# Kernel tuning notes

Measured on AMD Instinct MI355X. Metric: run time of the kernel, lower is better.

The kernel has to match this reference:

```python
import jax, jax.numpy as jnp
import numpy as np

N_NODES = 100000


def _gin_layer(x, edge_index, Wa, ba, Wb, bb):
    # GINConv, eps=0: h_i = MLP(x_i + sum_{j->i} x_j)
    src, dst = edge_index[0], edge_index[1]
    agg = jax.ops.segment_sum(x[src], dst, num_segments=N_NODES)  # [N, d]
    h = x + agg
    h = jax.nn.relu(h @ Wa + ba) @ Wb + bb
    return h


def setup_inputs() -> dict:
    key = jax.random.key(0)
    ks = jax.random.split(key, 8)
    d_in, d_h, E = 128, 128, 1600000
    scale_in = 1.0 / np.sqrt(d_in)
    scale_h = 1.0 / np.sqrt(d_h)
    return {
        "x": jax.random.normal(ks[0], (N_NODES, d_in), dtype=jnp.float32),
        "edge_index": jax.random.randint(ks[1], (2, E), 0, N_NODES, dtype=jnp.int64),
        "batch": jnp.zeros((N_NODES,), dtype=jnp.int64),
        "W1a": jax.random.normal(ks[2], (d_in, d_h), dtype=jnp.float32) * scale_in,
        "b1a": jnp.zeros((d_h,), dtype=jnp.float32),
        "W1b": jax.random.normal(ks[3], (d_h, d_h), dtype=jnp.float32) * scale_h,
        "b1b": jnp.zeros((d_h,), dtype=jnp.float32),
        "W2a": jax.random.normal(ks[4], (d_h, d_h), dtype=jnp.float32) * scale_h,
        "b2a": jnp.zeros((d_h,), dtype=jnp.float32),
        "W2b": jax.random.normal(ks[5], (d_h, d_h), dtype=jnp.float32) * scale_h,
        "b2b": jnp.zeros((d_h,), dtype=jnp.float32),
    }


def reference(x, edge_index, batch, W1a, b1a, W1b, b1b, W2a, b2a, W2b, b2b):
    h = jax.nn.relu(_gin_layer(x, edge_index, W1a, b1a, W1b, b1b))
    h = jax.nn.relu(_gin_layer(h, edge_index, W2a, b2a, W2b, b2b))
    return h
```

## Files before the change

### kernel.cpp

```cpp
#include <hip/hip_runtime.h>
#include <hip/hip_bf16.h>

#define D 128
#define EPB 4096
#define CAP 6144

typedef float f32x4 __attribute__((ext_vector_type(4)));
typedef float f32x2 __attribute__((ext_vector_type(2)));
typedef short short8 __attribute__((ext_vector_type(8)));


__device__ __forceinline__ unsigned bf16_rtn_bits(float x) {
    unsigned u = __float_as_uint(x);
    return (u + 0x7fffu + ((u >> 16) & 1u)) >> 16;
}

__device__ __forceinline__ f32x2 pkadd(f32x2 a, f32x2 b) {
    f32x2 d;
    asm("v_pk_add_f32 %0, %1, %2" : "=v"(d) : "v"(a), "v"(b));
    return d;
}

__device__ __forceinline__ void addbf8p(f32x2* acc, uint4 v) {
    f32x2 p0 = {__uint_as_float(v.x << 16), __uint_as_float(v.x & 0xffff0000u)};
    f32x2 p1 = {__uint_as_float(v.y << 16), __uint_as_float(v.y & 0xffff0000u)};
    f32x2 p2 = {__uint_as_float(v.z << 16), __uint_as_float(v.z & 0xffff0000u)};
    f32x2 p3 = {__uint_as_float(v.w << 16), __uint_as_float(v.w & 0xffff0000u)};
    acc[0] = pkadd(acc[0], p0);
    acc[1] = pkadd(acc[1], p1);
    acc[2] = pkadd(acc[2], p2);
    acc[3] = pkadd(acc[3], p3);
}


__global__ __launch_bounds__(256) void k_xtobf(const float4* __restrict__ X, uint4* __restrict__ O,
                                               int n8, int* __restrict__ gz, int nzero) {
    int i = blockIdx.x * 256 + threadIdx.x;
    if (i < nzero) gz[i] = 0;
    if (i >= n8) return;
    float4 a = X[2 * i], b = X[2 * i + 1];
    uint4 o;
    o.x = bf16_rtn_bits(a.x) | (bf16_rtn_bits(a.y) << 16);
    o.y = bf16_rtn_bits(a.z) | (bf16_rtn_bits(a.w) << 16);
    o.z = bf16_rtn_bits(b.x) | (bf16_rtn_bits(b.y) << 16);
    o.w = bf16_rtn_bits(b.z) | (bf16_rtn_bits(b.w) << 16);
    O[i] = o;
}

__global__ void k_wsplit4(const float* __restrict__ W1a, const float* __restrict__ W1b,
                          const float* __restrict__ W2a, const float* __restrict__ W2b,
                          unsigned short* __restrict__ Wt) {
    int m = blockIdx.x >> 6;
    int i = (blockIdx.x & 63) * 256 + threadIdx.x;
    const float* W = (m == 0) ? W1a : (m == 1) ? W1b : (m == 2) ? W2a : W2b;
    int k = i >> 7, n = i & 127;
    Wt[m * 16384 + n * 128 + k] = (unsigned short)bf16_rtn_bits(W[i]);
}


__global__ __launch_bounds__(256) void k_bin(const int* __restrict__ src,
                                             const int* __restrict__ dst, int E,
                                             int* __restrict__ gCursor,
                                             unsigned* __restrict__ binned) {
    __shared__ int cnt[512];
    __shared__ int offs[512];
    __shared__ int c2[512];
    __shared__ int gOff[512];
    __shared__ int s[256];
    __shared__ unsigned staged[EPB];
    __shared__ unsigned short bo[EPB];
    int t = threadIdx.x;
    cnt[t] = 0; cnt[t + 256] = 0;
    c2[t] = 0; c2[t + 256] = 0;
    __syncthreads();

    unsigned pk[EPB / 256];
    int bk[EPB / 256];
    int e0 = blockIdx.x * EPB;
#pragma unroll
    for (int i = 0; i < EPB / 256; ++i) {
        int e = e0 + i * 256 + t;
        int b = -1; unsigned p = 0;
        if (e < E) {
            int dv = dst[e], sv = src[e];
            b = dv >> 8;
            p = ((unsigned)sv << 8) | (unsigned)(dv & 255);
            atomicAdd(&cnt[b], 1);
        }
        pk[i] = p; bk[i] = b;
    }
    __syncthreads();
    int v0 = cnt[2 * t], v1 = cnt[2 * t + 1];
    int ps = v0 + v1;
    s[t] = ps;
    __syncthreads();
    for (int off = 1; off < 256; off <<= 1) {
        int tv = (t >= off) ? s[t - off] : 0;
        __syncthreads();
        s[t] += tv;
        __syncthreads();
    }
    int ex = s[t] - ps;
    offs[2 * t] = ex;
    offs[2 * t + 1] = ex + v0;
    if (cnt[2 * t])     gOff[2 * t]     = atomicAdd(&gCursor[2 * t], cnt[2 * t]);
    if (cnt[2 * t + 1]) gOff[2 * t + 1] = atomicAdd(&gCursor[2 * t + 1], cnt[2 * t + 1]);
    __syncthreads();
#pragma unroll
    for (int i = 0; i < EPB / 256; ++i) {
        int b = bk[i];
        if (b >= 0) {
            int p = offs[b] + atomicAdd(&c2[b], 1);
            staged[p] = pk[i];
            bo[p] = (unsigned short)b;
        }
    }
    __syncthreads();
    int total = s[255];
    for (int p = t; p < total; p += 256) {
        int b = bo[p];
        binned[(size_t)b * CAP + gOff[b] + (p - offs[b])] = staged[p];
    }
}

__global__ __launch_bounds__(256) void k_csr(const unsigned* __restrict__ binned,
                                             const int* __restrict__ bucketCnt,
                                             int* __restrict__ alloc,
                                             int2* __restrict__ rowse,
                                             int* __restrict__ colA,
                                             int Nn) {
    __shared__ int hist[256], loc[256], cur[256], s[256];
    __shared__ int baseSh;
    int t = threadIdx.x, b = blockIdx.x;
    int n = bucketCnt[b];
    const unsigned* bp = binned + (size_t)b * CAP;
    hist[t] = 0; cur[t] = 0;
    __syncthreads();
    for (int i = t; i < n; i += 256) atomicAdd(&hist[bp[i] & 255u], 1);
    __syncthreads();
    int v = hist[t];
    s[t] = v;
    __syncthreads();
    for (int off = 1; off < 256; off <<= 1) {
        int tv = (t >= off) ? s[t - off] : 0;
        __syncthreads();
        s[t] += tv;
        __syncthreads();
    }
    loc[t] = s[t] - v;
    if (t == 255) baseSh = atomicAdd(alloc, s[255]);
    __syncthreads();
    int base = baseSh;
    int node = b * 256 + t;
    if (node < Nn) rowse[node] = make_int2(base + loc[t], base + loc[t] + v);
    for (int i = t; i < n; i += 256) {
        unsigned w = bp[i];
        int dl = (int)(w & 255u);
        int p = atomicAdd(&cur[dl], 1);
        colA[base + loc[dl] + p] = (int)(w >> 8);
    }
}


__global__ __launch_bounds__(256) void agg_bf16(const unsigned short* __restrict__ X,
                                                const int2* __restrict__ rowse,
                                                const int* __restrict__ colA,
                                                unsigned short* __restrict__ H, int nnodes) {
    int node = blockIdx.x * 4 + (threadIdx.x >> 6);
    if (node >= nnodes) return;
    int lane = threadIdx.x & 63;
    int qt = lane >> 4, slot = lane & 15;
    const uint4* x4 = (const uint4*)X;
    size_t base = (size_t)node * 16 + slot;

    int2 se = rowse[node];
    int e = se.x, end = se.y;

    f32x2 acc[4] = {{0.f, 0.f}, {0.f, 0.f}, {0.f, 0.f}, {0.f, 0.f}};
    f32x2 acc2[4] = {{0.f, 0.f}, {0.f, 0.f}, {0.f, 0.f}, {0.f, 0.f}};
    if (qt == 0) addbf8p(acc, x4[base]);

    for (; e + 16 <= end; e += 16) {
        int s0 = colA[e + qt];
        int s1 = colA[e + 4 + qt];
        int s2 = colA[e + 8 + qt];
        int s3 = colA[e + 12 + qt];
        uint4 v0 = x4[(size_t)s0 * 16 + slot];
        uint4 v1 = x4[(size_t)s1 * 16 + slot];
        uint4 v2 = x4[(size_t)s2 * 16 + slot];
        uint4 v3 = x4[(size_t)s3 * 16 + slot];
        addbf8p(acc, v0);
        addbf8p(acc2, v1);
        addbf8p(acc, v2);
        addbf8p(acc2, v3);
    }
    if (e + 8 <= end) {
        int s0 = colA[e + qt];
        int s1 = colA[e + 4 + qt];
        uint4 v0 = x4[(size_t)s0 * 16 + slot];
        uint4 v1 = x4[(size_t)s1 * 16 + slot];
        addbf8p(acc, v0);
        addbf8p(acc2, v1);
        e += 8;
    }
    for (; e < end; e += 4) {
        int idx = e + qt;
        if (idx < end) {
            int s = colA[idx];
            addbf8p(acc, x4[(size_t)s * 16 + slot]);
        }
    }
    float a8[8];
#pragma unroll
    for (int j = 0; j < 4; ++j) {
        f32x2 t = pkadd(acc[j], acc2[j]);
        a8[2 * j] = t[0];
        a8[2 * j + 1] = t[1];
    }
#pragma unroll
    for (int j = 0; j < 8; ++j) {
        a8[j] += __shfl_xor(a8[j], 16);
        a8[j] += __shfl_xor(a8[j], 32);
    }
    if (qt == 0) {
        uint4 o;
        o.x = bf16_rtn_bits(a8[0]) | (bf16_rtn_bits(a8[1]) << 16);
        o.y = bf16_rtn_bits(a8[2]) | (bf16_rtn_bits(a8[3]) << 16);
        o.z = bf16_rtn_bits(a8[4]) | (bf16_rtn_bits(a8[5]) << 16);
        o.w = bf16_rtn_bits(a8[6]) | (bf16_rtn_bits(a8[7]) << 16);
        ((uint4*)H)[base] = o;
    }
}


template <bool OUT_BF16>
__global__ __launch_bounds__(256) void mlp_mfma(const unsigned short* __restrict__ Hb,
                                                const unsigned short* __restrict__ WaT,
                                                const float* __restrict__ ba,
                                                const unsigned short* __restrict__ WbT,
                                                const float* __restrict__ bb,
                                                void* __restrict__ OutP, int nrows) {
    __shared__ unsigned short sh[64 * 128];
    const int tid = threadIdx.x;
    const int wv = tid >> 6, l = tid & 63, q = l >> 4, cl = l & 15;
    const int ntiles = (nrows + 63) >> 6;

    short8 B1[2][4], B2[2][4];
    float bva[2], bvb[2];
#pragma unroll
    for (int cf = 0; cf < 2; ++cf) {
        const unsigned short* wa = WaT + (size_t)(wv * 32 + cf * 16 + cl) * 128 + q * 8;
        const unsigned short* wb = WbT + (size_t)(wv * 32 + cf * 16 + cl) * 128 + q * 8;
#pragma unroll
        for (int kk = 0; kk < 4; ++kk) {
            B1[cf][kk] = *(const short8*)(wa + kk * 32);
            B2[cf][kk] = *(const short8*)(wb + kk * 32);
        }
        bva[cf] = ba[wv * 32 + cf * 16 + cl];
        bvb[cf] = bb[wv * 32 + cf * 16 + cl];
    }

    for (int tile = blockIdx.x; tile < ntiles; tile += gridDim.x) {
        const int rows0 = tile * 64;
        const int nvalid = min(64, nrows - rows0);

        {
            const uint4* src = (const uint4*)(Hb + (size_t)rows0 * 128);
#pragma unroll
            for (int it = 0; it < 4; ++it) {
                int idx = it * 256 + tid;
                int row = idx >> 4, s16 = idx & 15;
                uint4 v = {0u, 0u, 0u, 0u};
                if (row < nvalid) v = src[idx];
                int byteoff = (row << 8) + ((s16 << 4) ^ ((row & 7) << 4));
                *(uint4*)((char*)sh + byteoff) = v;
            }
        }
        __syncthreads();

        f32x4 acc[4][2];
#pragma unroll
        for (int cf = 0; cf < 2; ++cf) {
            f32x4 a = {bva[cf], bva[cf], bva[cf], bva[cf]};
#pragma unroll
            for (int m = 0; m < 4; ++m) acc[m][cf] = a;
        }
#pragma unroll
        for (int kk = 0; kk < 4; ++kk) {
            short8 a[4];
#pragma unroll
            for (int m = 0; m < 4; ++m) {
                int row = m * 16 + cl;
                int byteoff = (row << 8) + ((kk * 64 + q * 16) ^ ((row & 7) << 4));
                a[m] = *(const short8*)((const char*)sh + byteoff);
            }
#pragma unroll
            for (int m = 0; m < 4; ++m)
#pragma unroll
                for (int cf = 0; cf < 2; ++cf)
                    acc[m][cf] = __builtin_amdgcn_mfma_f32_16x16x32_bf16(a[m], B1[cf][kk], acc[m][cf], 0, 0, 0);
        }
        __syncthreads();

#pragma unroll
        for (int m = 0; m < 4; ++m)
#pragma unroll
            for (int cf = 0; cf < 2; ++cf)
#pragma unroll
                for (int r = 0; r < 4; ++r) {
                    int row = m * 16 + q * 4 + r;
                    int col = wv * 32 + cf * 16 + cl;
                    int byteoff = (row << 8) + ((col * 2) ^ ((row & 7) << 4));
                    *(unsigned short*)((char*)sh + byteoff) =
                        (unsigned short)bf16_rtn_bits(fmaxf(acc[m][cf][r], 0.f));
                }
        __syncthreads();

#pragma unroll
        for (int cf = 0; cf < 2; ++cf) {
            f32x4 a = {bvb[cf], bvb[cf], bvb[cf], bvb[cf]};
#pragma unroll
            for (int m = 0; m < 4; ++m) acc[m][cf] = a;
        }
#pragma unroll
        for (int kk = 0; kk < 4; ++kk) {
            short8 a[4];
#pragma unroll
            for (int m = 0; m < 4; ++m) {
                int row = m * 16 + cl;
                int byteoff = (row << 8) + ((kk * 64 + q * 16) ^ ((row & 7) << 4));
                a[m] = *(const short8*)((const char*)sh + byteoff);
            }
#pragma unroll
            for (int m = 0; m < 4; ++m)
#pragma unroll
                for (int cf = 0; cf < 2; ++cf)
                    acc[m][cf] = __builtin_amdgcn_mfma_f32_16x16x32_bf16(a[m], B2[cf][kk], acc[m][cf], 0, 0, 0);
        }

#pragma unroll
        for (int m = 0; m < 4; ++m)
#pragma unroll
            for (int cf = 0; cf < 2; ++cf)
#pragma unroll
                for (int r = 0; r < 4; ++r) {
                    int row = m * 16 + q * 4 + r;
                    if (row < nvalid) {
                        float v = fmaxf(acc[m][cf][r], 0.f);
                        size_t gi = ((size_t)rows0 + row) * 128 + wv * 32 + cf * 16 + cl;
                        if (OUT_BF16)
                            ((unsigned short*)OutP)[gi] = (unsigned short)bf16_rtn_bits(v);
                        else
                            ((float*)OutP)[gi] = v;
                    }
                }
        __syncthreads();
    }
}


extern "C" void kernel_launch(void* const* d_in, const int* in_sizes, int n_in,
                              void* d_out, int out_size, void* d_ws, size_t ws_size,
                              hipStream_t stream) {
    const float* x  = (const float*)d_in[0];
    const int*   ei = (const int*)d_in[1];
    const float* W1a = (const float*)d_in[3];
    const float* b1a = (const float*)d_in[4];
    const float* W1b = (const float*)d_in[5];
    const float* b1b = (const float*)d_in[6];
    const float* W2a = (const float*)d_in[7];
    const float* b2a = (const float*)d_in[8];
    const float* W2b = (const float*)d_in[9];
    const float* b2b = (const float*)d_in[10];
    float* out = (float*)d_out;

    const int Nn = in_sizes[0] / D;
    const int E  = in_sizes[1] / 2;
    const int* srcIdx = ei;
    const int* dstIdx = ei + E;
    const int NB = (Nn + 255) >> 8;

    char* w = (char*)d_ws;
    size_t off = 0;
    int2* rowse = (int2*)(w + off);    off += (size_t)Nn * 8;
    off = (off + 255) & ~(size_t)255;
    int* gCursor = (int*)(w + off);    off += (size_t)(NB + 1) * 4;
    int* alloc = gCursor + NB;
    off = (off + 255) & ~(size_t)255;
    int* colA = (int*)(w + off);       off += (size_t)E * 4;
    off = (off + 255) & ~(size_t)255;
    unsigned short* wsp = (unsigned short*)(w + off); off += (size_t)4 * 16384 * 2;
    off = (off + 255) & ~(size_t)255;
    unsigned short* bufA = (unsigned short*)(w + off); off += (size_t)Nn * 128 * 2;
    off = (off + 255) & ~(size_t)255;
    unsigned short* bufB = (unsigned short*)(w + off);
    unsigned* binned = (unsigned*)bufB;

    unsigned short* W1aT = wsp + 0 * 16384;
    unsigned short* W1bT = wsp + 1 * 16384;
    unsigned short* W2aT = wsp + 2 * 16384;
    unsigned short* W2bT = wsp + 3 * 16384;

    const int gBin = (E + EPB - 1) / EPB;

    k_xtobf<<<(Nn * 16 + 255) / 256, 256, 0, stream>>>((const float4*)x, (uint4*)bufA,
                                                       Nn * 16, gCursor, NB + 1);
    k_wsplit4<<<256, 256, 0, stream>>>(W1a, W1b, W2a, W2b, wsp);

    k_bin<<<gBin, 256, 0, stream>>>(srcIdx, dstIdx, E, gCursor, binned);
    k_csr<<<NB, 256, 0, stream>>>(binned, gCursor, alloc, rowse, colA, Nn);

    const int gAgg = (Nn + 3) / 4;
    const int gMlp = 512;

    agg_bf16<<<gAgg, 256, 0, stream>>>(bufA, rowse, colA, bufB, Nn);
    mlp_mfma<true><<<gMlp, 256, 0, stream>>>(bufB, W1aT, b1a, W1bT, b1b, (void*)bufA, Nn);
    agg_bf16<<<gAgg, 256, 0, stream>>>(bufA, rowse, colA, bufB, Nn);
    mlp_mfma<false><<<gMlp, 256, 0, stream>>>(bufB, W2aT, b2a, W2bT, b2b, (void*)out, Nn);
}
```

Measured before the change: 225.7 us.

## Merge prep kernels and double-buffer MLP tile loads through registers

Folds the weight transpose/convert kernel into the x-to-bf16 conversion kernel so one launch replaces two. In the MLP kernel, each block now prefetches the next tile's rows into registers while computing the current tile, then writes them to a second shared-memory buffer. This hides global load latency and removes one barrier per tile. The cost is doubled LDS use (32 KB per block) and extra registers, which may lower occupancy.

```diff
diff --git a/kernel.cpp b/kernel.cpp
--- a/kernel.cpp
+++ b/kernel.cpp
@@ -33,9 +33,20 @@
 }
 
 
-__global__ __launch_bounds__(256) void k_xtobf(const float4* __restrict__ X, uint4* __restrict__ O,
-                                               int n8, int* __restrict__ gz, int nzero) {
-    int i = blockIdx.x * 256 + threadIdx.x;
+__global__ __launch_bounds__(256) void k_prep(const float* __restrict__ W1a, const float* __restrict__ W1b,
+                                              const float* __restrict__ W2a, const float* __restrict__ W2b,
+                                              unsigned short* __restrict__ Wt,
+                                              const float4* __restrict__ X, uint4* __restrict__ O,
+                                              int n8, int* __restrict__ gz, int nzero) {
+    if (blockIdx.x < 256) {
+        int m = blockIdx.x >> 6;
+        int i = (blockIdx.x & 63) * 256 + threadIdx.x;
+        const float* W = (m == 0) ? W1a : (m == 1) ? W1b : (m == 2) ? W2a : W2b;
+        int k = i >> 7, n = i & 127;
+        Wt[m * 16384 + n * 128 + k] = (unsigned short)bf16_rtn_bits(W[i]);
+        return;
+    }
+    int i = (blockIdx.x - 256) * 256 + threadIdx.x;
     if (i < nzero) gz[i] = 0;
     if (i >= n8) return;
     float4 a = X[2 * i], b = X[2 * i + 1];
@@ -45,16 +56,6 @@
     o.z = bf16_rtn_bits(b.x) | (bf16_rtn_bits(b.y) << 16);
     o.w = bf16_rtn_bits(b.z) | (bf16_rtn_bits(b.w) << 16);
     O[i] = o;
-}
-
-__global__ void k_wsplit4(const float* __restrict__ W1a, const float* __restrict__ W1b,
-                          const float* __restrict__ W2a, const float* __restrict__ W2b,
-                          unsigned short* __restrict__ Wt) {
-    int m = blockIdx.x >> 6;
-    int i = (blockIdx.x & 63) * 256 + threadIdx.x;
-    const float* W = (m == 0) ? W1a : (m == 1) ? W1b : (m == 2) ? W2a : W2b;
-    int k = i >> 7, n = i & 127;
-    Wt[m * 16384 + n * 128 + k] = (unsigned short)bf16_rtn_bits(W[i]);
 }
 
 
@@ -240,7 +241,7 @@
                                                 const unsigned short* __restrict__ WbT,
                                                 const float* __restrict__ bb,
                                                 void* __restrict__ OutP, int nrows) {
-    __shared__ unsigned short sh[64 * 128];
+    __shared__ unsigned short sh[2][64 * 128];
     const int tid = threadIdx.x;
     const int wv = tid >> 6, l = tid & 63, q = l >> 4, cl = l & 15;
     const int ntiles = (nrows + 63) >> 6;
@@ -260,24 +261,48 @@
         bvb[cf] = bb[wv * 32 + cf * 16 + cl];
     }
 
-    for (int tile = blockIdx.x; tile < ntiles; tile += gridDim.x) {
+    int tile = blockIdx.x;
+    if (tile >= ntiles) return;
+
+    {
         const int rows0 = tile * 64;
         const int nvalid = min(64, nrows - rows0);
-
-        {
-            const uint4* src = (const uint4*)(Hb + (size_t)rows0 * 128);
+        const uint4* src = (const uint4*)(Hb + (size_t)rows0 * 128);
+#pragma unroll
+        for (int it = 0; it < 4; ++it) {
+            int idx = it * 256 + tid;
+            int row = idx >> 4, s16 = idx & 15;
+            uint4 v = {0u, 0u, 0u, 0u};
+            if (row < nvalid) v = src[idx];
+            int byteoff = (row << 8) + ((s16 << 4) ^ ((row & 7) << 4));
+            *(uint4*)((char*)&sh[0][0] + byteoff) = v;
+        }
+    }
+    int cur = 0;
+    __syncthreads();
+
+    while (true) {
+        const int rows0 = tile * 64;
+        const int nvalid = min(64, nrows - rows0);
+        const int nexttile = tile + (int)gridDim.x;
+        const bool havenext = nexttile < ntiles;
+
+        uint4 r[4];
+        if (havenext) {
+            const int nr0 = nexttile * 64;
+            const int nnv = min(64, nrows - nr0);
+            const uint4* src = (const uint4*)(Hb + (size_t)nr0 * 128);
 #pragma unroll
             for (int it = 0; it < 4; ++it) {
                 int idx = it * 256 + tid;
-                int row = idx >> 4, s16 = idx & 15;
+                int row = idx >> 4;
                 uint4 v = {0u, 0u, 0u, 0u};
-                if (row < nvalid) v = src[idx];
-                int byteoff = (row << 8) + ((s16 << 4) ^ ((row & 7) << 4));
-                *(uint4*)((char*)sh + byteoff) = v;
+                if (row < nnv) v = src[idx];
+                r[it] = v;
             }
         }
-        __syncthreads();
-
+
+        const char* shc = (const char*)&sh[cur][0];
         f32x4 acc[4][2];
 #pragma unroll
         for (int cf = 0; cf < 2; ++cf) {
@@ -292,7 +317,7 @@
             for (int m = 0; m < 4; ++m) {
                 int row = m * 16 + cl;
                 int byteoff = (row << 8) + ((kk * 64 + q * 16) ^ ((row & 7) << 4));
-                a[m] = *(const short8*)((const char*)sh + byteoff);
+                a[m] = *(const short8*)(shc + byteoff);
             }
 #pragma unroll
             for (int m = 0; m < 4; ++m)
@@ -307,12 +332,12 @@
 #pragma unroll
             for (int cf = 0; cf < 2; ++cf)
 #pragma unroll
-                for (int r = 0; r < 4; ++r) {
-                    int row = m * 16 + q * 4 + r;
+                for (int rr = 0; rr < 4; ++rr) {
+                    int row = m * 16 + q * 4 + rr;
                     int col = wv * 32 + cf * 16 + cl;
                     int byteoff = (row << 8) + ((col * 2) ^ ((row & 7) << 4));
-                    *(unsigned short*)((char*)sh + byteoff) =
-                        (unsigned short)bf16_rtn_bits(fmaxf(acc[m][cf][r], 0.f));
+                    *(unsigned short*)((char*)&sh[cur][0] + byteoff) =
+                        (unsigned short)bf16_rtn_bits(fmaxf(acc[m][cf][rr], 0.f));
                 }
         __syncthreads();
 
@@ -329,7 +354,7 @@
             for (int m = 0; m < 4; ++m) {
                 int row = m * 16 + cl;
                 int byteoff = (row << 8) + ((kk * 64 + q * 16) ^ ((row & 7) << 4));
-                a[m] = *(const short8*)((const char*)sh + byteoff);
+                a[m] = *(const short8*)(shc + byteoff);
             }
 #pragma unroll
             for (int m = 0; m < 4; ++m)
@@ -343,10 +368,10 @@
 #pragma unroll
             for (int cf = 0; cf < 2; ++cf)
 #pragma unroll
-                for (int r = 0; r < 4; ++r) {
-                    int row = m * 16 + q * 4 + r;
+                for (int rr = 0; rr < 4; ++rr) {
+                    int row = m * 16 + q * 4 + rr;
                     if (row < nvalid) {
-                        float v = fmaxf(acc[m][cf][r], 0.f);
+                        float v = fmaxf(acc[m][cf][rr], 0.f);
                         size_t gi = ((size_t)rows0 + row) * 128 + wv * 32 + cf * 16 + cl;
                         if (OUT_BF16)
                             ((unsigned short*)OutP)[gi] = (unsigned short)bf16_rtn_bits(v);
@@ -354,7 +379,18 @@
                             ((float*)OutP)[gi] = v;
                     }
                 }
-        __syncthreads();
+
+        if (!havenext) break;
+#pragma unroll
+        for (int it = 0; it < 4; ++it) {
+            int idx = it * 256 + tid;
+            int row = idx >> 4, s16 = idx & 15;
+            int byteoff = (row << 8) + ((s16 << 4) ^ ((row & 7) << 4));
+            *(uint4*)((char*)&sh[cur ^ 1][0] + byteoff) = r[it];
+        }
+        __syncthreads();
+        cur ^= 1;
+        tile = nexttile;
     }
 }
 
@@ -402,10 +438,10 @@
     unsigned short* W2bT = wsp + 3 * 16384;
 
     const int gBin = (E + EPB - 1) / EPB;
-
-    k_xtobf<<<(Nn * 16 + 255) / 256, 256, 0, stream>>>((const float4*)x, (uint4*)bufA,
-                                                       Nn * 16, gCursor, NB + 1);
-    k_wsplit4<<<256, 256, 0, stream>>>(W1a, W1b, W2a, W2b, wsp);
+    const int gPrep = 256 + (Nn * 16 + 255) / 256;
+
+    k_prep<<<gPrep, 256, 0, stream>>>(W1a, W1b, W2a, W2b, wsp,
+                                      (const float4*)x, (uint4*)bufA, Nn * 16, gCursor, NB + 1);
 
     k_bin<<<gBin, 256, 0, stream>>>(srcIdx, dstIdx, E, gCursor, binned);
     k_csr<<<NB, 256, 0, stream>>>(binned, gCursor, alloc, rowse, colA, Nn);
```

New measurement: 218.1 us (median of 2 runs). 1.03x faster.
